# Kernel optimization log

Measured on AMD Instinct MI355X. Metric: run time of the kernel, lower is better.

## Reference

```python
import jax, jax.numpy as jnp
import numpy as np

B, C, H, W = 8, 512, 64, 64


def setup_inputs() -> dict:
    key = jax.random.key(0)
    k1, k2, k3, k4 = jax.random.split(key, 4)
    x = jax.random.normal(k1, (B, C, H, W), dtype=jnp.float32)
    spatial_feat = jax.random.normal(k2, (B, C, H, W), dtype=jnp.float32)
    multi_scale_feat = jax.random.normal(k3, (B, C, H, W), dtype=jnp.float32)
    scale = jnp.array(1.0, dtype=jnp.float32)  # nn.Parameter(torch.tensor(1.0))
    conv_w = jax.random.normal(k4, (C, C), dtype=jnp.float32) * 0.02  # 1x1 conv kernel [out,in]
    conv_b = jnp.zeros((C,), dtype=jnp.float32)
    return {"x": x, "spatial_feat": spatial_feat, "multi_scale_feat": multi_scale_feat,
            "scale": scale, "conv_w": conv_w, "conv_b": conv_b}


def reference(x, spatial_feat, multi_scale_feat, scale, conv_w, conv_b):
    Bq, Cq, Hq, Wq = x.shape
    L = Hq * Wq
    query = x.reshape(Bq, Cq, L)                                   # [B,C,L]
    kv = jnp.concatenate([spatial_feat.reshape(Bq, Cq, L),
                          multi_scale_feat.reshape(Bq, Cq, L)], axis=1)  # [B,2C,L]
    # attn = scale * L^-0.5 * (query @ kv^T), channel attention [B,C,2C]
    attn = jnp.einsum('bcl,bkl->bck', query, kv) * (scale * (float(L) ** -0.5))
    attn = jax.nn.softmax(attn, axis=-1)
    fused = jnp.einsum('bck,bkl->bcl', attn, kv).reshape(Bq, Cq, Hq, Wq)  # [B,C,H,W]
    out = jnp.einsum('oc,bchw->bohw', conv_w, fused) + conv_b[None, :, None, None]
    return out
```

## Files before the change

### kernel.cpp

```cpp
#include <hip/hip_runtime.h>

#define Bq   8
#define Cc   512
#define Ll   4096
#define KV2  1024
#define KS   4
#define KSL  (Ll / KS)

typedef _Float16 f16;
typedef __attribute__((ext_vector_type(4))) _Float16 f16x4;
typedef __attribute__((ext_vector_type(8))) _Float16 f16x8;
typedef __attribute__((ext_vector_type(4))) float    f32x4;

typedef const __attribute__((address_space(1))) void* gas_t;
typedef __attribute__((address_space(3))) void*       las_t;

__device__ __forceinline__ void gl16(const f16* g, f16* l) {
    __builtin_amdgcn_global_load_lds((gas_t)g, (las_t)l, 16, 0, 0);
}

__global__ __launch_bounds__(256) void p_cvt(const float* __restrict__ in,
                                             f16* __restrict__ hi, int n4) {
    int i = blockIdx.x * 256 + threadIdx.x;
    if (i >= n4) return;
    float4 v = ((const float4*)in)[i];
    f16x4 hv; hv[0] = (f16)v.x; hv[1] = (f16)v.y; hv[2] = (f16)v.z; hv[3] = (f16)v.w;
    ((f16x4*)hi)[i] = hv;
}

__global__ __launch_bounds__(256) void p_split(const float* __restrict__ in,
                                               f16* __restrict__ hi,
                                               f16* __restrict__ lo, int n4) {
    int i = blockIdx.x * 256 + threadIdx.x;
    if (i >= n4) return;
    float4 v = ((const float4*)in)[i];
    f16 h0 = (f16)v.x, h1 = (f16)v.y, h2 = (f16)v.z, h3 = (f16)v.w;
    f16x4 hv; hv[0] = h0; hv[1] = h1; hv[2] = h2; hv[3] = h3;
    f16x4 lv;
    lv[0] = (f16)(v.x - (float)h0); lv[1] = (f16)(v.y - (float)h1);
    lv[2] = (f16)(v.z - (float)h2); lv[3] = (f16)(v.w - (float)h3);
    ((f16x4*)hi)[i] = hv;
    ((f16x4*)lo)[i] = lv;
}

__global__ __launch_bounds__(256) void p_kv(const float* __restrict__ sp,
                                            const float* __restrict__ ms,
                                            f16* __restrict__ kvhi,
                                            f16* __restrict__ kvt) {
    __shared__ __align__(16) f16 tile[64][72];
    const int b = blockIdx.z, c0 = blockIdx.y * 64, l0 = blockIdx.x * 64;
    const int t = threadIdx.x;
    const int r = t >> 2, q = t & 3;
    const float* src = (c0 + r < Cc)
        ? sp + ((size_t)b * Cc + c0 + r) * Ll
        : ms + ((size_t)b * Cc + (c0 + r - Cc)) * Ll;
    f16 h[16];
    #pragma unroll
    for (int i = 0; i < 4; ++i) {
        float4 v = *(const float4*)(src + l0 + q * 16 + i * 4);
        h[i * 4 + 0] = (f16)v.x; h[i * 4 + 1] = (f16)v.y;
        h[i * 4 + 2] = (f16)v.z; h[i * 4 + 3] = (f16)v.w;
    }
    {
        f16* dst = &kvhi[((size_t)b * KV2 + c0 + r) * Ll + l0 + q * 16];
        *(f16x8*)dst       = *(const f16x8*)&h[0];
        *(f16x8*)(dst + 8) = *(const f16x8*)&h[8];
    }
    #pragma unroll
    for (int e = 0; e < 16; ++e)
        tile[q * 16 + e][r] = h[e];
    __syncthreads();
    const int lr_ = t >> 3, g = t & 7;
    #pragma unroll
    for (int p = 0; p < 2; ++p) {
        const int l = lr_ + 32 * p;
        f16x8 o = *(const f16x8*)&tile[l][g * 8];
        *(f16x8*)&kvt[((size_t)b * Ll + l0 + l) * KV2 + c0 + g * 8] = o;
    }
}

template<int KD, int NBN, int EPI, int KSV>
__global__ __launch_bounds__(512, 2) void gemm256(
    const f16* __restrict__ Ah, size_t sAb, int lda,
    const f16* __restrict__ Bh, size_t sBb, int ldb,
    const float* __restrict__ scale_ptr, const float* __restrict__ bias,
    float* __restrict__ Cf, f16* __restrict__ Chi,
    size_t sCb, size_t sliceC, int ldc)
{
    constexpr int NT = KD / 64;
    __shared__ __align__(16) f16 ring[8][128 * 64];

    int wg = blockIdx.x;
    const int chunk = (int)gridDim.x >> 3;
    wg = (wg & 7) * chunk + (wg >> 3);
    const int m0 = (wg & 1) * 256; wg >>= 1;
    const int n0 = (wg % NBN) * 256; wg /= NBN;
    const int b = wg / KSV, s = wg % KSV;

    const int t = threadIdx.x;
    const int w = t >> 6, lane = t & 63;
    const int quad = lane >> 4, lr = lane & 15;
    const int wm = (w >> 2) * 128, wn = (w & 3) * 64;
    const int tA = 2 + (w >> 2);
    const int tB = (w & 3) >> 1;
    const int brow = (w & 1) * 64;
    const int srow = lane >> 3, sslot = (lane & 7) ^ srow;
    const int x7 = lr & 7;

    const f16* gA = Ah + (size_t)b * sAb + (size_t)s * KD
                  + (size_t)(m0 + w * 8 + srow) * lda + sslot * 8;
    const f16* gB = Bh + (size_t)b * sBb + (size_t)s * KD
                  + (size_t)(n0 + w * 8 + srow) * ldb + sslot * 8;
    f16* const ld0 = &ring[0][0] + (w * 8) * 64;

    auto stA = [&](int tile, int half) {
        if (tile >= NT) return;
        f16* d = ld0 + ((tile * 4 + 2 + half) & 7) * (128 * 64);
        const f16* g = gA + (size_t)(half * 128) * lda + tile * 64;
        gl16(g, d);
        gl16(g + (size_t)64 * lda, d + 64 * 64);
    };
    auto stB = [&](int tile, int half) {
        if (tile >= NT) return;
        f16* d = ld0 + ((tile * 4 + half) & 7) * (128 * 64);
        const f16* g = gB + (size_t)(half * 128) * ldb + tile * 64;
        gl16(g, d);
        gl16(g + (size_t)64 * ldb, d + 64 * 64);
    };

    f32x4 acc[8][4];
    #pragma unroll
    for (int i = 0; i < 8; ++i)
        #pragma unroll
        for (int j = 0; j < 4; ++j) {
            acc[i][j][0] = 0.f; acc[i][j][1] = 0.f;
            acc[i][j][2] = 0.f; acc[i][j][3] = 0.f;
        }

    stB(0, 0); stB(0, 1); stA(0, 0); stA(0, 1);
    stB(1, 0); stB(1, 1); stA(1, 0);
    asm volatile("s_waitcnt vmcnt(6)" ::: "memory");
    __builtin_amdgcn_s_barrier();

    f16x8 a[4][2], bf[4][2];

    #pragma unroll 2
    for (int T = 0; T < NT; ++T) {
        const f16* sAp = &ring[(T * 4 + tA) & 7][0];
        const f16* sBp = &ring[(T * 4 + tB) & 7][0];

        #pragma unroll
        for (int ii = 0; ii < 4; ++ii)
            #pragma unroll
            for (int ks = 0; ks < 2; ++ks)
                a[ii][ks] = *(const f16x8*)&sAp[(ii * 16 + lr) * 64
                             + ((((ks << 2) | quad) ^ x7) << 3)];
        #pragma unroll
        for (int j = 0; j < 4; ++j)
            #pragma unroll
            for (int ks = 0; ks < 2; ++ks)
                bf[j][ks] = *(const f16x8*)&sBp[(brow + j * 16 + lr) * 64
                             + ((((ks << 2) | quad) ^ x7) << 3)];
        stA(T + 1, 1);
        asm volatile("s_waitcnt lgkmcnt(0)" ::: "memory");
        __builtin_amdgcn_s_barrier();
        __builtin_amdgcn_s_setprio(1);
        #pragma unroll
        for (int ii = 0; ii < 4; ++ii)
            #pragma unroll
            for (int j = 0; j < 2; ++j)
                #pragma unroll
                for (int ks = 0; ks < 2; ++ks)
                    acc[ii][j] = __builtin_amdgcn_mfma_f32_16x16x32_f16(
                                     a[ii][ks], bf[j][ks], acc[ii][j], 0, 0, 0);
        __builtin_amdgcn_s_setprio(0);
        __builtin_amdgcn_s_barrier();

        stB(T + 2, 0);
        __builtin_amdgcn_s_barrier();
        __builtin_amdgcn_s_setprio(1);
        #pragma unroll
        for (int ii = 0; ii < 4; ++ii)
            #pragma unroll
            for (int j = 0; j < 2; ++j)
                #pragma unroll
                for (int ks = 0; ks < 2; ++ks)
                    acc[ii][2 + j] = __builtin_amdgcn_mfma_f32_16x16x32_f16(
                                     a[ii][ks], bf[2 + j][ks], acc[ii][2 + j], 0, 0, 0);
        __builtin_amdgcn_s_setprio(0);
        __builtin_amdgcn_s_barrier();

        #pragma unroll
        for (int ii = 0; ii < 4; ++ii)
            #pragma unroll
            for (int ks = 0; ks < 2; ++ks)
                a[ii][ks] = *(const f16x8*)&sAp[((ii + 4) * 16 + lr) * 64
                             + ((((ks << 2) | quad) ^ x7) << 3)];
        stB(T + 2, 1);
        asm volatile("s_waitcnt lgkmcnt(0)" ::: "memory");
        __builtin_amdgcn_s_barrier();
        __builtin_amdgcn_s_setprio(1);
        #pragma unroll
        for (int ii = 0; ii < 4; ++ii)
            #pragma unroll
            for (int j = 0; j < 2; ++j)
                #pragma unroll
                for (int ks = 0; ks < 2; ++ks)
                    acc[4 + ii][j] = __builtin_amdgcn_mfma_f32_16x16x32_f16(
                                     a[ii][ks], bf[j][ks], acc[4 + ii][j], 0, 0, 0);
        __builtin_amdgcn_s_setprio(0);
        __builtin_amdgcn_s_barrier();

        stA(T + 2, 0);
        if (T + 2 < NT) { asm volatile("s_waitcnt vmcnt(6)" ::: "memory"); }
        else            { asm volatile("s_waitcnt vmcnt(0)" ::: "memory"); }
        __builtin_amdgcn_s_barrier();
        __builtin_amdgcn_s_setprio(1);
        #pragma unroll
        for (int ii = 0; ii < 4; ++ii)
            #pragma unroll
            for (int j = 0; j < 2; ++j)
                #pragma unroll
                for (int ks = 0; ks < 2; ++ks)
                    acc[4 + ii][2 + j] = __builtin_amdgcn_mfma_f32_16x16x32_f16(
                                     a[ii][ks], bf[2 + j][ks], acc[4 + ii][2 + j], 0, 0, 0);
        __builtin_amdgcn_s_setprio(0);
        __builtin_amdgcn_s_barrier();
    }

    if constexpr (EPI == 0) {
        const float alpha = scale_ptr[0] * 0.015625f;
        f16* Cs = Chi + (size_t)s * sliceC + (size_t)b * sCb;
        #pragma unroll
        for (int i = 0; i < 8; ++i)
            #pragma unroll
            for (int j = 0; j < 4; ++j) {
                const int n = n0 + wn + j * 16 + lr;
                #pragma unroll
                for (int r = 0; r < 4; ++r) {
                    const int m = m0 + wm + i * 16 + quad * 4 + r;
                    Cs[(size_t)m * ldc + n] = (f16)(alpha * acc[i][j][r]);
                }
            }
    } else {
        float* Co = Cf + (size_t)b * sCb;
        #pragma unroll
        for (int i = 0; i < 8; ++i)
            #pragma unroll
            for (int j = 0; j < 4; ++j) {
                const int n = n0 + wn + j * 16 + lr;
                #pragma unroll
                for (int r = 0; r < 4; ++r) {
                    const int m = m0 + wm + i * 16 + quad * 4 + r;
                    Co[(size_t)m * ldc + n] = acc[i][j][r] + bias[m];
                }
            }
    }
}

template<int KD, int NBN, int EPI, bool LO, int KSV>
__global__ __launch_bounds__(256, 3) void gemm_mfma(
    const f16* __restrict__ Ah, const f16* __restrict__ Al, size_t sAb, int lda,
    const f16* __restrict__ Bh, size_t sBb, int ldb,
    const float* __restrict__ scale_ptr, const float* __restrict__ bias,
    float* __restrict__ Cf, f16* __restrict__ Chi,
    size_t sCb, size_t sliceC, int ldc)
{
    __shared__ __align__(16) f16 sA[128 * 64];
    __shared__ __align__(16) f16 sB[128 * 64];
    __shared__ __align__(16) f16 sL[LO ? 128 * 64 : 8];

    int wg = blockIdx.x;
    const int chunk = (int)gridDim.x >> 3;
    wg = (wg & 7) * chunk + (wg >> 3);
    const int m0 = (wg & 3) * 128; wg >>= 2;
    const int n0 = (wg % NBN) * 128; wg /= NBN;
    const int b  = wg / KSV, s = wg % KSV;

    const int t = threadIdx.x;
    const int w = t >> 6, lane = t & 63;
    const int quad = lane >> 4, lr = lane & 15;
    const int wm = (w & 1) * 64, wn = (w >> 1) * 64;
    const int sr = lane >> 3, sc = lane & 7;
    const int swb = (sc ^ sr) << 3;
    const int x7 = lr & 7;

    const f16* gA = Ah + (size_t)b * sAb + (size_t)s * KD
                  + (size_t)(m0 + w * 8 + sr) * lda + swb;
    const f16* gB = Bh + (size_t)b * sBb + (size_t)s * KD
                  + (size_t)(n0 + w * 8 + sr) * ldb + swb;
    const f16* gL = LO ? (Al + (size_t)(m0 + w * 8 + sr) * lda + swb) : nullptr;

    f32x4 acc[4][4];
    #pragma unroll
    for (int i = 0; i < 4; ++i)
        #pragma unroll
        for (int j = 0; j < 4; ++j) {
            acc[i][j][0] = 0.f; acc[i][j][1] = 0.f;
            acc[i][j][2] = 0.f; acc[i][j][3] = 0.f;
        }

    for (int k0 = 0; k0 < KD; k0 += 64) {
        #pragma unroll
        for (int i = 0; i < 4; ++i) {
            gl16(gA + k0 + (size_t)(i * 32) * lda, &sA[(i * 32 + w * 8) * 64]);
            gl16(gB + k0 + (size_t)(i * 32) * ldb, &sB[(i * 32 + w * 8) * 64]);
            if constexpr (LO)
                gl16(gL + k0 + (size_t)(i * 32) * lda, &sL[(i * 32 + w * 8) * 64]);
        }
        asm volatile("s_waitcnt vmcnt(0)" ::: "memory");
        __syncthreads();
        #pragma unroll
        for (int ks = 0; ks < 2; ++ks) {
            f16x8 af[4], bfr[4];
            #pragma unroll
            for (int i = 0; i < 4; ++i)
                af[i] = *(const f16x8*)&sA[(wm + i * 16 + lr) * 64
                         + ((((ks << 2) | quad) ^ x7) << 3)];
            #pragma unroll
            for (int j = 0; j < 4; ++j)
                bfr[j] = *(const f16x8*)&sB[(wn + j * 16 + lr) * 64
                         + ((((ks << 2) | quad) ^ x7) << 3)];
            #pragma unroll
            for (int i = 0; i < 4; ++i)
                #pragma unroll
                for (int j = 0; j < 4; ++j)
                    acc[i][j] = __builtin_amdgcn_mfma_f32_16x16x32_f16(
                                    af[i], bfr[j], acc[i][j], 0, 0, 0);
            if constexpr (LO) {
                f16x8 lf[4];
                #pragma unroll
                for (int i = 0; i < 4; ++i)
                    lf[i] = *(const f16x8*)&sL[(wm + i * 16 + lr) * 64
                             + ((((ks << 2) | quad) ^ x7) << 3)];
                #pragma unroll
                for (int i = 0; i < 4; ++i)
                    #pragma unroll
                    for (int j = 0; j < 4; ++j)
                        acc[i][j] = __builtin_amdgcn_mfma_f32_16x16x32_f16(
                                        lf[i], bfr[j], acc[i][j], 0, 0, 0);
            }
        }
        __syncthreads();
    }

    if constexpr (EPI == 0) {
        const float alpha = scale_ptr[0] * 0.015625f;
        f16* Cs = Chi + (size_t)s * sliceC + (size_t)b * sCb;
        #pragma unroll
        for (int i = 0; i < 4; ++i)
            #pragma unroll
            for (int j = 0; j < 4; ++j) {
                const int n = n0 + wn + j * 16 + lr;
                #pragma unroll
                for (int r = 0; r < 4; ++r) {
                    const int m = m0 + wm + i * 16 + quad * 4 + r;
                    Cs[(size_t)m * ldc + n] = (f16)(alpha * acc[i][j][r]);
                }
            }
    } else if constexpr (EPI == 1) {
        f16* Cs = Chi + (size_t)b * sCb;
        #pragma unroll
        for (int i = 0; i < 4; ++i)
            #pragma unroll
            for (int j = 0; j < 4; ++j) {
                const int n = n0 + wn + j * 16 + lr;
                #pragma unroll
                for (int r = 0; r < 4; ++r) {
                    const int m = m0 + wm + i * 16 + quad * 4 + r;
                    Cs[(size_t)m * ldc + n] = (f16)acc[i][j][r];
                }
            }
    } else {
        float* Co = Cf + (size_t)b * sCb;
        #pragma unroll
        for (int i = 0; i < 4; ++i)
            #pragma unroll
            for (int j = 0; j < 4; ++j) {
                const int n = n0 + wn + j * 16 + lr;
                #pragma unroll
                for (int r = 0; r < 4; ++r) {
                    const int m = m0 + wm + i * 16 + quad * 4 + r;
                    Co[(size_t)m * ldc + n] = acc[i][j][r] + bias[m];
                }
            }
    }
}

__global__ __launch_bounds__(256) void k2_softmax_t(const f16* __restrict__ attnP,
                                                    f16* __restrict__ attnT) {
    __shared__ float rmax[16], rinv[16];
    __shared__ __align__(16) f16 tile[16][68];
    const int b = blockIdx.y, c0 = blockIdx.x * 16;
    const int t = threadIdx.x, w = t >> 6, lane = t & 63;
    const size_t sS = (size_t)Bq * Cc * KV2;

    for (int rr = 0; rr < 4; ++rr) {
        const int r = w * 4 + rr;
        const f16* base = attnP + ((size_t)b * Cc + c0 + r) * KV2;
        float v[16];
        #pragma unroll
        for (int i = 0; i < 2; ++i) {
            f16x8 u = *(const f16x8*)(base + (lane + 64 * i) * 8);
            #pragma unroll
            for (int j = 0; j < 8; ++j) v[i * 8 + j] = (float)u[j];
        }
        #pragma unroll
        for (int s = 1; s < KS; ++s) {
            const f16* bs = base + (size_t)s * sS;
            #pragma unroll
            for (int i = 0; i < 2; ++i) {
                f16x8 u = *(const f16x8*)(bs + (lane + 64 * i) * 8);
                #pragma unroll
                for (int j = 0; j < 8; ++j) v[i * 8 + j] += (float)u[j];
            }
        }
        float m = -3.4e38f;
        #pragma unroll
        for (int i = 0; i < 16; ++i) m = fmaxf(m, v[i]);
        #pragma unroll
        for (int off = 32; off; off >>= 1) m = fmaxf(m, __shfl_xor(m, off));
        float s = 0.f;
        #pragma unroll
        for (int i = 0; i < 16; ++i) s += __expf(v[i] - m);
        #pragma unroll
        for (int off = 32; off; off >>= 1) s += __shfl_xor(s, off);
        if (lane == 0) { rmax[r] = m; rinv[r] = 1.0f / s; }
    }
    __syncthreads();

    const int r2 = t >> 4, cn = (t & 15) * 4;
    const int n4 = t >> 2, q = t & 3;
    for (int nt = 0; nt < 16; ++nt) {
        const f16* base = attnP + ((size_t)b * Cc + c0 + r2) * KV2 + nt * 64 + cn;
        float vx[4];
        {
            f16x4 u = *(const f16x4*)base;
            #pragma unroll
            for (int j = 0; j < 4; ++j) vx[j] = (float)u[j];
        }
        #pragma unroll
        for (int s = 1; s < KS; ++s) {
            f16x4 u = *(const f16x4*)(base + (size_t)s * sS);
            #pragma unroll
            for (int j = 0; j < 4; ++j) vx[j] += (float)u[j];
        }
        const float m = rmax[r2], iv = rinv[r2];
        f16x4 hv;
        hv[0] = (f16)(__expf(vx[0] - m) * iv); hv[1] = (f16)(__expf(vx[1] - m) * iv);
        hv[2] = (f16)(__expf(vx[2] - m) * iv); hv[3] = (f16)(__expf(vx[3] - m) * iv);
        *(f16x4*)&tile[r2][cn] = hv;
        __syncthreads();
        f16x4 o;
        o[0] = tile[q * 4 + 0][n4]; o[1] = tile[q * 4 + 1][n4];
        o[2] = tile[q * 4 + 2][n4]; o[3] = tile[q * 4 + 3][n4];
        *(f16x4*)&attnT[((size_t)b * KV2 + nt * 64 + n4) * Cc + c0 + q * 4] = o;
        __syncthreads();
    }
}

#define BM 64
#define BN 64
#define BK 32
#define PAD 4

__device__ __forceinline__ const float* kv_row(const float* __restrict__ sp,
                                               const float* __restrict__ ms,
                                               int b, int k) {
    return (k < Cc) ? (sp + ((size_t)b * Cc + k) * Ll)
                    : (ms + ((size_t)b * Cc + (k - Cc)) * Ll);
}

__global__ __launch_bounds__(256) void k1_logits(const float* __restrict__ x,
                                                 const float* __restrict__ sp,
                                                 const float* __restrict__ ms,
                                                 const float* __restrict__ scale,
                                                 float* __restrict__ attn) {
    __shared__ __align__(16) float As[BK][BM + PAD];
    __shared__ __align__(16) float Bs[BK][BN + PAD];
    const int b = blockIdx.z, m0 = blockIdx.y * BM, n0 = blockIdx.x * BN;
    const int t = threadIdx.x, tx = t & 15, ty = t >> 4, q = t & 7, r = t >> 3;
    const float alpha = scale[0] * (1.0f / 64.0f);
    const float* Abase = x + (size_t)b * Cc * Ll;
    float acc[4][4] = {};
    for (int k0 = 0; k0 < Ll; k0 += BK) {
        #pragma unroll
        for (int hh = 0; hh < 2; ++hh) {
            const int rw = r + 32 * hh;
            float4 v = *(const float4*)(Abase + (size_t)(m0 + rw) * Ll + k0 + 4 * q);
            As[4*q+0][rw] = v.x; As[4*q+1][rw] = v.y; As[4*q+2][rw] = v.z; As[4*q+3][rw] = v.w;
        }
        #pragma unroll
        for (int hh = 0; hh < 2; ++hh) {
            const int rw = r + 32 * hh;
            const float* Brow = kv_row(sp, ms, b, n0 + rw);
            float4 v = *(const float4*)(Brow + k0 + 4 * q);
            Bs[4*q+0][rw] = v.x; Bs[4*q+1][rw] = v.y; Bs[4*q+2][rw] = v.z; Bs[4*q+3][rw] = v.w;
        }
        __syncthreads();
        #pragma unroll
        for (int k = 0; k < BK; ++k) {
            float a[4], bb[4];
            *(float4*)a  = *(const float4*)&As[k][4 * ty];
            *(float4*)bb = *(const float4*)&Bs[k][4 * tx];
            #pragma unroll
            for (int i = 0; i < 4; ++i)
                #pragma unroll
                for (int j = 0; j < 4; ++j) acc[i][j] += a[i] * bb[j];
        }
        __syncthreads();
    }
    #pragma unroll
    for (int i = 0; i < 4; ++i) {
        const int m = m0 + 4 * ty + i;
        float4 o;
        o.x = alpha * acc[i][0]; o.y = alpha * acc[i][1];
        o.z = alpha * acc[i][2]; o.w = alpha * acc[i][3];
        *(float4*)(attn + ((size_t)b * Cc + m) * KV2 + n0 + 4 * tx) = o;
    }
}

__global__ __launch_bounds__(256) void k2_softmax(float* __restrict__ attn) {
    float* p = attn + (size_t)blockIdx.x * KV2;
    const int t = threadIdx.x, lane = t & 63, wv = t >> 6;
    float4 v = ((const float4*)p)[t];
    float m = fmaxf(fmaxf(v.x, v.y), fmaxf(v.z, v.w));
    #pragma unroll
    for (int off = 32; off; off >>= 1) m = fmaxf(m, __shfl_down(m, off));
    __shared__ float redm[4];
    if (lane == 0) redm[wv] = m;
    __syncthreads();
    m = fmaxf(fmaxf(redm[0], redm[1]), fmaxf(redm[2], redm[3]));
    v.x = __expf(v.x - m); v.y = __expf(v.y - m);
    v.z = __expf(v.z - m); v.w = __expf(v.w - m);
    float s = v.x + v.y + v.z + v.w;
    #pragma unroll
    for (int off = 32; off; off >>= 1) s += __shfl_down(s, off);
    __shared__ float reds[4];
    if (lane == 0) reds[wv] = s;
    __syncthreads();
    s = reds[0] + reds[1] + reds[2] + reds[3];
    const float inv = 1.0f / s;
    v.x *= inv; v.y *= inv; v.z *= inv; v.w *= inv;
    ((float4*)p)[t] = v;
}

__global__ __launch_bounds__(256) void k3_wattn(const float* __restrict__ W,
                                                const float* __restrict__ attn,
                                                float* __restrict__ attn2) {
    __shared__ __align__(16) float As[BK][BM + PAD];
    __shared__ __align__(16) float Bs[BK][BN];
    const int b = blockIdx.z, m0 = blockIdx.y * BM, n0 = blockIdx.x * BN;
    const int t = threadIdx.x, tx = t & 15, ty = t >> 4;
    const int q = t & 7, r = t >> 3, c4 = t & 15, kr = t >> 4;
    const float* Bbase = attn + (size_t)b * Cc * KV2;
    float acc[4][4] = {};
    for (int k0 = 0; k0 < Cc; k0 += BK) {
        #pragma unroll
        for (int hh = 0; hh < 2; ++hh) {
            const int rw = r + 32 * hh;
            float4 v = *(const float4*)(W + (size_t)(m0 + rw) * Cc + k0 + 4 * q);
            As[4*q+0][rw] = v.x; As[4*q+1][rw] = v.y; As[4*q+2][rw] = v.z; As[4*q+3][rw] = v.w;
        }
        #pragma unroll
        for (int hh = 0; hh < 2; ++hh) {
            const int k = kr + 16 * hh;
            float4 v = *(const float4*)(Bbase + (size_t)(k0 + k) * KV2 + n0 + 4 * c4);
            *(float4*)&Bs[k][4 * c4] = v;
        }
        __syncthreads();
        #pragma unroll
        for (int k = 0; k < BK; ++k) {
            float a[4], bb[4];
            *(float4*)a  = *(const float4*)&As[k][4 * ty];
            *(float4*)bb = *(const float4*)&Bs[k][4 * tx];
            #pragma unroll
            for (int i = 0; i < 4; ++i)
                #pragma unroll
                for (int j = 0; j < 4; ++j) acc[i][j] += a[i] * bb[j];
        }
        __syncthreads();
    }
    #pragma unroll
    for (int i = 0; i < 4; ++i) {
        const int m = m0 + 4 * ty + i;
        float4 o;
        o.x = acc[i][0]; o.y = acc[i][1]; o.z = acc[i][2]; o.w = acc[i][3];
        *(float4*)(attn2 + ((size_t)b * Cc + m) * KV2 + n0 + 4 * tx) = o;
    }
}

__global__ __launch_bounds__(256) void k4_out(const float* __restrict__ attn2,
                                              const float* __restrict__ sp,
                                              const float* __restrict__ ms,
                                              const float* __restrict__ bias,
                                              float* __restrict__ out) {
    __shared__ __align__(16) float As[BK][BM + PAD];
    __shared__ __align__(16) float Bs[BK][BN];
    const int b = blockIdx.z, m0 = blockIdx.y * BM, n0 = blockIdx.x * BN;
    const int t = threadIdx.x, tx = t & 15, ty = t >> 4;
    const int q = t & 7, r = t >> 3, c4 = t & 15, kr = t >> 4;
    const float* Abase = attn2 + (size_t)b * Cc * KV2;
    float acc[4][4] = {};
    for (int k0 = 0; k0 < KV2; k0 += BK) {
        #pragma unroll
        for (int hh = 0; hh < 2; ++hh) {
            const int rw = r + 32 * hh;
            float4 v = *(const float4*)(Abase + (size_t)(m0 + rw) * KV2 + k0 + 4 * q);
            As[4*q+0][rw] = v.x; As[4*q+1][rw] = v.y; As[4*q+2][rw] = v.z; As[4*q+3][rw] = v.w;
        }
        #pragma unroll
        for (int hh = 0; hh < 2; ++hh) {
            const int k = kr + 16 * hh;
            const float* Brow = kv_row(sp, ms, b, k0 + k);
            float4 v = *(const float4*)(Brow + n0 + 4 * c4);
            *(float4*)&Bs[k][4 * c4] = v;
        }
        __syncthreads();
        #pragma unroll
        for (int k = 0; k < BK; ++k) {
            float a[4], bb[4];
            *(float4*)a  = *(const float4*)&As[k][4 * ty];
            *(float4*)bb = *(const float4*)&Bs[k][4 * tx];
            #pragma unroll
            for (int i = 0; i < 4; ++i)
                #pragma unroll
                for (int j = 0; j < 4; ++j) acc[i][j] += a[i] * bb[j];
        }
        __syncthreads();
    }
    #pragma unroll
    for (int i = 0; i < 4; ++i) {
        const int m = m0 + 4 * ty + i;
        const float bm = bias[m];
        float4 o;
        o.x = acc[i][0] + bm; o.y = acc[i][1] + bm;
        o.z = acc[i][2] + bm; o.w = acc[i][3] + bm;
        *(float4*)(out + ((size_t)b * Cc + m) * Ll + n0 + 4 * tx) = o;
    }
}

extern "C" void kernel_launch(void* const* d_in, const int* in_sizes, int n_in,
                              void* d_out, int out_size, void* d_ws, size_t ws_size,
                              hipStream_t stream) {
    const float* x     = (const float*)d_in[0];
    const float* sp    = (const float*)d_in[1];
    const float* ms    = (const float*)d_in[2];
    const float* scale = (const float*)d_in[3];
    const float* W     = (const float*)d_in[4];
    const float* bias  = (const float*)d_in[5];
    float* out = (float*)d_out;

    const size_t NEED = 219152384;
    if (ws_size >= NEED) {
        char* ws = (char*)d_ws;
        f16* attnP = (f16*)ws;
        f16* Xhi   = (f16*)(ws + 33554432);
        f16* KVhi  = (f16*)(ws + 67108864);
        f16* KVT   = (f16*)(ws + 134217728);
        f16* Whi   = (f16*)(ws + 201326592);
        f16* Wlo   = (f16*)(ws + 201850880);
        f16* attnT = (f16*)(ws + 202375168);
        f16* A2hi  = (f16*)(ws + 210763776);

        dim3 blk(256);
        p_cvt  <<<dim3(16384),                 blk, 0, stream>>>(x, Xhi, Bq * Cc * Ll / 4);
        p_kv   <<<dim3(Ll / 64, KV2 / 64, Bq), blk, 0, stream>>>(sp, ms, KVhi, KVT);
        p_split<<<dim3(256),                   blk, 0, stream>>>(W, Whi, Wlo, Cc * Cc / 4);

        gemm256<KSL, KV2 / 256, 0, KS>
            <<<dim3(2 * (KV2 / 256) * Bq * KS), dim3(512), 0, stream>>>(
            Xhi, (size_t)Cc * Ll, Ll,
            KVhi, (size_t)KV2 * Ll, Ll,
            scale, nullptr, nullptr, attnP,
            (size_t)Cc * KV2, (size_t)Bq * Cc * KV2, KV2);

        k2_softmax_t<<<dim3(Cc / 16, Bq), blk, 0, stream>>>(attnP, attnT);

        gemm_mfma<Cc, KV2 / 128, 1, true, 1>
            <<<dim3(4 * (KV2 / 128) * Bq), blk, 0, stream>>>(
            Whi, Wlo, (size_t)0, Cc,
            attnT, (size_t)KV2 * Cc, Cc,
            nullptr, nullptr, nullptr, A2hi,
            (size_t)Cc * KV2, (size_t)0, KV2);

        gemm256<KV2, Ll / 256, 2, 1>
            <<<dim3(2 * (Ll / 256) * Bq), dim3(512), 0, stream>>>(
            A2hi, (size_t)Cc * KV2, KV2,
            KVT, (size_t)Ll * KV2, KV2,
            nullptr, bias, out, nullptr,
            (size_t)Cc * Ll, (size_t)0, Ll);
    } else {
        float* attn  = (float*)d_ws;
        float* attn2 = attn + (size_t)Bq * Cc * KV2;
        dim3 blk(256);
        k1_logits <<<dim3(KV2 / BN, Cc / BM, Bq), blk, 0, stream>>>(x, sp, ms, scale, attn);
        k2_softmax<<<dim3(Bq * Cc),               blk, 0, stream>>>(attn);
        k3_wattn  <<<dim3(KV2 / BN, Cc / BM, Bq), blk, 0, stream>>>(W, attn, attn2);
        k4_out    <<<dim3(Ll / BN, Cc / BM, Bq), blk, 0, stream>>>(attn2, sp, ms, bias, out);
    }
}
```

Baseline: 346.5 us.

## Pipeline KV conversion over four L-tiles and single-pass softmax transpose

The p_kv kernel now processes four 64-wide L tiles per block, prefetching the next tile's fp32 loads into registers while converting and transposing the current one. It uses a double-buffered, XOR-swizzled LDS tile so reads and writes avoid bank conflicts and only one barrier is needed per tile. k2_softmax_t now keeps the normalized probabilities for all 16 rows in a 64KB swizzled LDS buffer. This removes the second read of the four split-K partial slices and the per-tile barrier loop, but the large shared allocation lowers occupancy.

```diff
diff --git a/kernel.cpp b/kernel.cpp
--- a/kernel.cpp
+++ b/kernel.cpp
@@ -47,35 +47,55 @@
                                             const float* __restrict__ ms,
                                             f16* __restrict__ kvhi,
                                             f16* __restrict__ kvt) {
-    __shared__ __align__(16) f16 tile[64][72];
-    const int b = blockIdx.z, c0 = blockIdx.y * 64, l0 = blockIdx.x * 64;
+    __shared__ __align__(16) f16 tile[2][64][72];
+    const int b = blockIdx.z, c0 = blockIdx.y * 64, lb = blockIdx.x * 256;
     const int t = threadIdx.x;
     const int r = t >> 2, q = t & 3;
     const float* src = (c0 + r < Cc)
         ? sp + ((size_t)b * Cc + c0 + r) * Ll
         : ms + ((size_t)b * Cc + (c0 + r - Cc)) * Ll;
-    f16 h[16];
-    #pragma unroll
-    for (int i = 0; i < 4; ++i) {
-        float4 v = *(const float4*)(src + l0 + q * 16 + i * 4);
-        h[i * 4 + 0] = (f16)v.x; h[i * 4 + 1] = (f16)v.y;
-        h[i * 4 + 2] = (f16)v.z; h[i * 4 + 3] = (f16)v.w;
-    }
-    {
+    const int lr_ = t >> 3, g = t & 7;
+    const int rw = r ^ (q << 4);
+
+    float4 va[4], vb[4];
+    #pragma unroll
+    for (int i = 0; i < 4; ++i)
+        va[i] = *(const float4*)(src + lb + q * 16 + i * 4);
+
+    #pragma unroll
+    for (int it = 0; it < 4; ++it) {
+        const int l0 = lb + it * 64;
+        const int p = it & 1;
+        if (it < 3) {
+            #pragma unroll
+            for (int i = 0; i < 4; ++i)
+                vb[i] = *(const float4*)(src + l0 + 64 + q * 16 + i * 4);
+        }
+        f16 h[16];
+        #pragma unroll
+        for (int i = 0; i < 4; ++i) {
+            float4 v = va[i];
+            h[i * 4 + 0] = (f16)v.x; h[i * 4 + 1] = (f16)v.y;
+            h[i * 4 + 2] = (f16)v.z; h[i * 4 + 3] = (f16)v.w;
+        }
         f16* dst = &kvhi[((size_t)b * KV2 + c0 + r) * Ll + l0 + q * 16];
         *(f16x8*)dst       = *(const f16x8*)&h[0];
         *(f16x8*)(dst + 8) = *(const f16x8*)&h[8];
-    }
-    #pragma unroll
-    for (int e = 0; e < 16; ++e)
-        tile[q * 16 + e][r] = h[e];
-    __syncthreads();
-    const int lr_ = t >> 3, g = t & 7;
-    #pragma unroll
-    for (int p = 0; p < 2; ++p) {
-        const int l = lr_ + 32 * p;
-        f16x8 o = *(const f16x8*)&tile[l][g * 8];
-        *(f16x8*)&kvt[((size_t)b * Ll + l0 + l) * KV2 + c0 + g * 8] = o;
+        #pragma unroll
+        for (int e = 0; e < 16; ++e)
+            tile[p][q * 16 + e][rw] = h[e];
+        asm volatile("s_waitcnt lgkmcnt(0)" ::: "memory");
+        __builtin_amdgcn_s_barrier();
+        #pragma unroll
+        for (int pp = 0; pp < 2; ++pp) {
+            const int l = lr_ + 32 * pp;
+            f16x8 o = *(const f16x8*)&tile[p][l][(g * 8) ^ (l & 48)];
+            *(f16x8*)&kvt[((size_t)b * Ll + l0 + l) * KV2 + c0 + g * 8] = o;
+        }
+        if (it < 3) {
+            #pragma unroll
+            for (int i = 0; i < 4; ++i) va[i] = vb[i];
+        }
     }
 }
 
@@ -389,12 +409,12 @@
 
 __global__ __launch_bounds__(256) void k2_softmax_t(const f16* __restrict__ attnP,
                                                     f16* __restrict__ attnT) {
-    __shared__ float rmax[16], rinv[16];
-    __shared__ __align__(16) f16 tile[16][68];
+    __shared__ __align__(16) float rowe[16][1024];
     const int b = blockIdx.y, c0 = blockIdx.x * 16;
     const int t = threadIdx.x, w = t >> 6, lane = t & 63;
     const size_t sS = (size_t)Bq * Cc * KV2;
 
+    #pragma unroll
     for (int rr = 0; rr < 4; ++rr) {
         const int r = w * 4 + rr;
         const f16* base = attnP + ((size_t)b * Cc + c0 + r) * KV2;
@@ -421,41 +441,37 @@
         #pragma unroll
         for (int off = 32; off; off >>= 1) m = fmaxf(m, __shfl_xor(m, off));
         float s = 0.f;
-        #pragma unroll
-        for (int i = 0; i < 16; ++i) s += __expf(v[i] - m);
+        float e[16];
+        #pragma unroll
+        for (int i = 0; i < 16; ++i) { e[i] = __expf(v[i] - m); s += e[i]; }
         #pragma unroll
         for (int off = 32; off; off >>= 1) s += __shfl_xor(s, off);
-        if (lane == 0) { rmax[r] = m; rinv[r] = 1.0f / s; }
+        const float iv = 1.0f / s;
+        #pragma unroll
+        for (int i = 0; i < 2; ++i)
+            #pragma unroll
+            for (int j4 = 0; j4 < 2; ++j4) {
+                const int g = (lane + 64 * i) * 2 + j4;
+                const int gs = g ^ ((g >> 3) & 7);
+                float4 o;
+                o.x = e[i * 8 + j4 * 4 + 0] * iv; o.y = e[i * 8 + j4 * 4 + 1] * iv;
+                o.z = e[i * 8 + j4 * 4 + 2] * iv; o.w = e[i * 8 + j4 * 4 + 3] * iv;
+                *(float4*)&rowe[r][gs * 4] = o;
+            }
     }
     __syncthreads();
 
-    const int r2 = t >> 4, cn = (t & 15) * 4;
-    const int n4 = t >> 2, q = t & 3;
-    for (int nt = 0; nt < 16; ++nt) {
-        const f16* base = attnP + ((size_t)b * Cc + c0 + r2) * KV2 + nt * 64 + cn;
-        float vx[4];
-        {
-            f16x4 u = *(const f16x4*)base;
-            #pragma unroll
-            for (int j = 0; j < 4; ++j) vx[j] = (float)u[j];
-        }
-        #pragma unroll
-        for (int s = 1; s < KS; ++s) {
-            f16x4 u = *(const f16x4*)(base + (size_t)s * sS);
-            #pragma unroll
-            for (int j = 0; j < 4; ++j) vx[j] += (float)u[j];
-        }
-        const float m = rmax[r2], iv = rinv[r2];
-        f16x4 hv;
-        hv[0] = (f16)(__expf(vx[0] - m) * iv); hv[1] = (f16)(__expf(vx[1] - m) * iv);
-        hv[2] = (f16)(__expf(vx[2] - m) * iv); hv[3] = (f16)(__expf(vx[3] - m) * iv);
-        *(f16x4*)&tile[r2][cn] = hv;
-        __syncthreads();
-        f16x4 o;
-        o[0] = tile[q * 4 + 0][n4]; o[1] = tile[q * 4 + 1][n4];
-        o[2] = tile[q * 4 + 2][n4]; o[3] = tile[q * 4 + 3][n4];
-        *(f16x4*)&attnT[((size_t)b * KV2 + nt * 64 + n4) * Cc + c0 + q * 4] = o;
-        __syncthreads();
+    const int half = t & 1;
+    #pragma unroll
+    for (int nt = 0; nt < 8; ++nt) {
+        const int n = nt * 128 + (t >> 1);
+        const int g = n >> 2, gs = g ^ ((g >> 3) & 7);
+        const int sc = gs * 4 + (n & 3);
+        f16x8 hv;
+        #pragma unroll
+        for (int cc = 0; cc < 8; ++cc)
+            hv[cc] = (f16)rowe[half * 8 + cc][sc];
+        *(f16x8*)&attnT[((size_t)b * KV2 + n) * Cc + c0 + half * 8] = hv;
     }
 }
 
@@ -664,9 +680,9 @@
         f16* A2hi  = (f16*)(ws + 210763776);
 
         dim3 blk(256);
-        p_cvt  <<<dim3(16384),                 blk, 0, stream>>>(x, Xhi, Bq * Cc * Ll / 4);
-        p_kv   <<<dim3(Ll / 64, KV2 / 64, Bq), blk, 0, stream>>>(sp, ms, KVhi, KVT);
-        p_split<<<dim3(256),                   blk, 0, stream>>>(W, Whi, Wlo, Cc * Cc / 4);
+        p_cvt  <<<dim3(16384),                  blk, 0, stream>>>(x, Xhi, Bq * Cc * Ll / 4);
+        p_kv   <<<dim3(Ll / 256, KV2 / 64, Bq), blk, 0, stream>>>(sp, ms, KVhi, KVT);
+        p_split<<<dim3(256),                    blk, 0, stream>>>(W, Whi, Wlo, Cc * Cc / 4);
 
         gemm256<KSL, KV2 / 256, 0, KS>
             <<<dim3(2 * (KV2 / 256) * Bq * KS), dim3(512), 0, stream>>>(
```

Result: faster. 338.8 us (-2.2%).
